# Performance work log

Measured on AMD Instinct MI355X. Metric: run time of the kernel, lower is better.

## Reference

```python
import jax, jax.numpy as jnp
import numpy as np

N_ACT = 300000
C = 128
K = 9
BATCH, H, W = 4, 1024, 1024
EPS = 1e-4  # scn BatchNormalization default eps


def _build_rulebook(rng):
    # sample N_ACT unique active sites on a (BATCH, H, W) grid
    flat = np.sort(rng.choice(BATCH * H * W, size=N_ACT, replace=False).astype(np.int64))
    b = flat // (H * W)
    y = (flat // W) % H
    x = flat % W
    nbr = np.full((N_ACT, K), -1, dtype=np.int32)
    k = 0
    for dy in (-1, 0, 1):
        for dx in (-1, 0, 1):
            ny, nx = y + dy, x + dx
            valid = (ny >= 0) & (ny < H) & (nx >= 0) & (nx < W)
            nflat = b * (H * W) + ny * W + nx
            pos = np.searchsorted(flat, nflat)
            pos_c = np.clip(pos, 0, N_ACT - 1)
            found = valid & (flat[pos_c] == nflat)
            nbr[:, k] = np.where(found, pos_c, -1).astype(np.int32)
            k += 1
    return jnp.asarray(nbr)


def setup_inputs() -> dict:
    key = jax.random.key(0)
    k1, k2, k3 = jax.random.split(key, 3)
    rng = np.random.default_rng(0)
    nbr_idx = _build_rulebook(rng)
    scale = 1.0 / np.sqrt(K * C)
    return {
        "x": jax.random.normal(k1, (N_ACT, C), dtype=jnp.float32),
        "nbr_idx": nbr_idx,
        "W1": jax.random.normal(k2, (K, C, C), dtype=jnp.float32) * scale,
        "gamma1": jnp.ones((C,), jnp.float32),
        "beta1": jnp.zeros((C,), jnp.float32),
        "W2": jax.random.normal(k3, (K, C, C), dtype=jnp.float32) * scale,
        "gamma2": jnp.ones((C,), jnp.float32),
        "beta2": jnp.zeros((C,), jnp.float32),
    }


def _subm_conv(feats, nbr_idx, Wk):
    # gather -> GEMM -> accumulate, one pass per kernel offset (K=9 fixed)
    out = jnp.zeros((feats.shape[0], Wk.shape[2]), feats.dtype)
    for k in range(Wk.shape[0]):
        idx = nbr_idx[:, k]
        mask = (idx >= 0)[:, None]
        g = jnp.where(mask, feats[jnp.maximum(idx, 0)], 0.0)
        out = out + g @ Wk[k]
    return out


def _batchnorm(feats, gamma, beta):
    mean = feats.mean(axis=0)
    var = feats.var(axis=0)  # biased, as in torch BN normalization
    return (feats - mean) * jax.lax.rsqrt(var + EPS) * gamma + beta


def reference(x, nbr_idx, W1, gamma1, beta1, W2, gamma2, beta2):
    out = _subm_conv(x, nbr_idx, W1)
    out = jax.nn.relu(_batchnorm(out, gamma1, beta1))  # BatchNormReLU
    out = _subm_conv(out, nbr_idx, W2)
    out = _batchnorm(out, gamma2, beta2)  # BatchNormalization
    return jax.nn.relu(out + x)  # AddTable + ReLU
```

## Files before the change

### kernel.cpp

```cpp
#include <hip/hip_runtime.h>


#define N_ACT 300000
#define NTAP  9
#define EPSV  1e-4f

using f16x8 = __attribute__((ext_vector_type(8))) _Float16;
using f32x4 = __attribute__((ext_vector_type(4))) float;

#define OFF_PH    0UL
#define OFF_TMP   76800000UL
#define OFF_W1    230400000UL
#define OFF_W2    (OFF_W1 + 294912UL)
#define OFF_STATS (OFF_W2 + 294912UL)
#define OFF_ZBUF  (OFF_STATS + 2048UL)
#define OFF_SB    (OFF_ZBUF + 256UL)

__device__ __forceinline__ unsigned short f2h(float v) {
  _Float16 h = (_Float16)v;
  return __builtin_bit_cast(unsigned short, h);
}

__global__ void prep_kernel(const float* __restrict__ W1, const float* __restrict__ W2,
                            unsigned short* __restrict__ w1, unsigned short* __restrict__ w2,
                            float* __restrict__ zstats) {
  int b = blockIdx.x, t = threadIdx.x;
  if (b == 36) {
    for (int i = t; i < 576; i += 256) zstats[i] = 0.f;
    return;
  }
  int w = b / 18, rem = b % 18;
  int tap = rem >> 1, ch = rem & 1;
  const float* W = w ? W2 : W1;
  unsigned short* o = w ? w2 : w1;
  int n  = t >> 1;
  int s0 = (t & 1) * 4;
  for (int s = s0; s < s0 + 4; ++s) {
    int sigma = s ^ (n & 7);
    for (int j = 0; j < 8; ++j) {
      int   k = ch * 64 + sigma * 8 + j;
      float v = W[tap * 16384 + k * 128 + n];
      o[rem * 8192 + n * 64 + s * 8 + j] = f2h(v);
    }
  }
}

__global__ void tohalf_kernel(const float* __restrict__ x, unsigned short* __restrict__ ph) {
  int i = (blockIdx.x * 256 + threadIdx.x) * 8;
  float4 a = *(const float4*)(x + i);
  float4 b = *(const float4*)(x + i + 4);
  uint4 p;
  p.x = (unsigned)f2h(a.x) | ((unsigned)f2h(a.y) << 16);
  p.y = (unsigned)f2h(a.z) | ((unsigned)f2h(a.w) << 16);
  p.z = (unsigned)f2h(b.x) | ((unsigned)f2h(b.y) << 16);
  p.w = (unsigned)f2h(b.z) | ((unsigned)f2h(b.w) << 16);
  *(uint4*)(ph + i) = p;
}

__global__ __launch_bounds__(256, 2)
void conv_kernel(const unsigned short* __restrict__ pH, const int* __restrict__ nbr,
                 const unsigned short* __restrict__ wH,
                 unsigned short* __restrict__ outp, float* __restrict__ ssum, float* __restrict__ ssq,
                 const unsigned short* __restrict__ zbuf) {
  __shared__ char smem[65536];
  const int t  = threadIdx.x;
  const int wv = t >> 6, ln = t & 63;
  const int m0 = blockIdx.x * 128;
  const int rs = ln >> 3, sg = ln & 7;
  const int lane16 = ln & 15, g = ln >> 4;

  int idx[NTAP][4];
#pragma unroll
  for (int tap = 0; tap < NTAP; ++tap)
#pragma unroll
    for (int it = 0; it < 4; ++it) {
      int gm = m0 + wv * 32 + it * 8 + rs;
      idx[tap][it] = (gm < N_ACT) ? nbr[gm * 9 + tap] : -1;
    }

  f32x4 acc[16];
#pragma unroll
  for (int i = 0; i < 16; ++i) acc[i] = f32x4{0.f, 0.f, 0.f, 0.f};

  auto stage = [&](int c, int p) {
    const int tap = c >> 1, ch = c & 1;
#pragma unroll
    for (int it = 0; it < 4; ++it) {
      int r     = wv * 32 + it * 8 + rs;
      int sigma = sg ^ (r & 7);
      int id    = idx[tap][it];
      long off  = (long)(id >= 0 ? id : 0) * 128 + ch * 64 + sigma * 8;
      const unsigned short* gs = (id >= 0) ? (pH + off) : (zbuf + sigma * 8);
      int lo = p * 16384 + r * 128 + sg * 16;
      __builtin_amdgcn_global_load_lds((const __attribute__((address_space(1))) void*)gs,
                                       (__attribute__((address_space(3))) void*)(smem + lo), 16, 0, 0);
    }
    const char* gb = (const char*)wH + (tap * 2 + ch) * 16384;
#pragma unroll
    for (int it = 0; it < 4; ++it) {
      int o = wv * 4096 + it * 1024 + ln * 16;
      __builtin_amdgcn_global_load_lds((const __attribute__((address_space(1))) void*)(gb + o),
                                       (__attribute__((address_space(3))) void*)(smem + 32768 + p * 16384 + o), 16, 0, 0);
    }
  };

  auto compute = [&](int p) {
    const char* bufA = smem + p * 16384;
    const char* bufB = smem + 32768 + p * 16384;
#pragma unroll
    for (int ks = 0; ks < 2; ++ks) {
      f16x8 ah[4], bh[4];
      int sigma = ks * 4 + g;
#pragma unroll
      for (int mt = 0; mt < 4; ++mt) {
        int m = (wv & 1) * 64 + mt * 16 + lane16;
        ah[mt] = *(const f16x8*)(bufA + m * 128 + ((sigma ^ (m & 7)) * 16));
      }
#pragma unroll
      for (int nt = 0; nt < 4; ++nt) {
        int n = (wv >> 1) * 64 + nt * 16 + lane16;
        bh[nt] = *(const f16x8*)(bufB + n * 128 + ((sigma ^ (n & 7)) * 16));
      }
#pragma unroll
      for (int mt = 0; mt < 4; ++mt)
#pragma unroll
        for (int nt = 0; nt < 4; ++nt)
          acc[mt * 4 + nt] = __builtin_amdgcn_mfma_f32_16x16x32_f16(ah[mt], bh[nt], acc[mt * 4 + nt], 0, 0, 0);
    }
  };

  stage(0, 0);
  asm volatile("s_waitcnt vmcnt(0)" ::: "memory");
  __builtin_amdgcn_sched_barrier(0);
  __builtin_amdgcn_s_barrier();

#pragma unroll
  for (int c = 0; c < 17; ++c) {
    stage(c + 1, (c + 1) & 1);
    compute(c & 1);
    asm volatile("s_waitcnt vmcnt(0)" ::: "memory");
    __builtin_amdgcn_sched_barrier(0);
    __builtin_amdgcn_s_barrier();
  }
  compute(1);

  int rowbase = m0 + (wv & 1) * 64;
  int colbase = (wv >> 1) * 64;
  float s[4], q[4];
#pragma unroll
  for (int nt = 0; nt < 4; ++nt) { s[nt] = 0.f; q[nt] = 0.f; }
#pragma unroll
  for (int mt = 0; mt < 4; ++mt)
#pragma unroll
    for (int nt = 0; nt < 4; ++nt)
#pragma unroll
      for (int r = 0; r < 4; ++r) {
        float v  = acc[mt * 4 + nt][r];
        int  row = rowbase + mt * 16 + g * 4 + r;
        int  col = colbase + nt * 16 + lane16;
        if (row < N_ACT) outp[row * 128 + col] = f2h(v);
        s[nt] += v; q[nt] += v * v;
      }
  __syncthreads();
  float* sbuf = (float*)smem;
  float* qbuf = ((float*)smem) + 256;
#pragma unroll
  for (int nt = 0; nt < 4; ++nt) {
    float sv = s[nt], qv = q[nt];
    sv += __shfl_xor(sv, 16, 64); sv += __shfl_xor(sv, 32, 64);
    qv += __shfl_xor(qv, 16, 64); qv += __shfl_xor(qv, 32, 64);
    if (ln < 16) { sbuf[wv * 64 + nt * 16 + ln] = sv; qbuf[wv * 64 + nt * 16 + ln] = qv; }
  }
  __syncthreads();
  if (t < 128) {
    int c = t;
    float tot = (c < 64) ? (sbuf[c] + sbuf[64 + c]) : (sbuf[128 + (c - 64)] + sbuf[192 + (c - 64)]);
    atomicAdd(ssum + c, tot);
  } else {
    int c = t - 128;
    float tot = (c < 64) ? (qbuf[c] + qbuf[64 + c]) : (qbuf[128 + (c - 64)] + qbuf[192 + (c - 64)]);
    atomicAdd(ssq + c, tot);
  }
}

__global__ void finalize_stats_kernel(const float* __restrict__ ssum, const float* __restrict__ ssq,
                                      const float* __restrict__ gamma, const float* __restrict__ beta,
                                      float* __restrict__ scale, float* __restrict__ bias) {
  int c = threadIdx.x;
  float mean = ssum[c] * (1.f / N_ACT);
  float var  = ssq[c] * (1.f / N_ACT) - mean * mean;
  float sc   = rsqrtf(var + EPSV) * gamma[c];
  scale[c] = sc;
  bias[c]  = beta[c] - mean * sc;
}

__global__ void bn_relu_tohalf_kernel(const unsigned short* __restrict__ tmp,
                                      const float* __restrict__ scale, const float* __restrict__ bias,
                                      unsigned short* __restrict__ ph) {
  int i = (blockIdx.x * 256 + threadIdx.x) * 8;
  int c = i & 127;
  f16x8 v = *(const f16x8*)(tmp + i);
  float4 s0 = *(const float4*)(scale + c);
  float4 s1 = *(const float4*)(scale + c + 4);
  float4 b0 = *(const float4*)(bias + c);
  float4 b1 = *(const float4*)(bias + c + 4);
  float y0 = fmaxf((float)v[0] * s0.x + b0.x, 0.f);
  float y1 = fmaxf((float)v[1] * s0.y + b0.y, 0.f);
  float y2 = fmaxf((float)v[2] * s0.z + b0.z, 0.f);
  float y3 = fmaxf((float)v[3] * s0.w + b0.w, 0.f);
  float y4 = fmaxf((float)v[4] * s1.x + b1.x, 0.f);
  float y5 = fmaxf((float)v[5] * s1.y + b1.y, 0.f);
  float y6 = fmaxf((float)v[6] * s1.z + b1.z, 0.f);
  float y7 = fmaxf((float)v[7] * s1.w + b1.w, 0.f);
  uint4 p;
  p.x = (unsigned)f2h(y0) | ((unsigned)f2h(y1) << 16);
  p.y = (unsigned)f2h(y2) | ((unsigned)f2h(y3) << 16);
  p.z = (unsigned)f2h(y4) | ((unsigned)f2h(y5) << 16);
  p.w = (unsigned)f2h(y6) | ((unsigned)f2h(y7) << 16);
  *(uint4*)(ph + i) = p;
}

__global__ void final_kernel(const unsigned short* __restrict__ tmp,
                             const float* __restrict__ scale, const float* __restrict__ bias,
                             const float* __restrict__ x, float* __restrict__ outp) {
  int i = (blockIdx.x * 256 + threadIdx.x) * 8;
  int c = i & 127;
  f16x8 v = *(const f16x8*)(tmp + i);
  float4 s0 = *(const float4*)(scale + c);
  float4 s1 = *(const float4*)(scale + c + 4);
  float4 b0 = *(const float4*)(bias + c);
  float4 b1 = *(const float4*)(bias + c + 4);
  float4 x0 = *(const float4*)(x + i);
  float4 x1 = *(const float4*)(x + i + 4);
  float4 o0, o1;
  o0.x = fmaxf((float)v[0] * s0.x + b0.x + x0.x, 0.f);
  o0.y = fmaxf((float)v[1] * s0.y + b0.y + x0.y, 0.f);
  o0.z = fmaxf((float)v[2] * s0.z + b0.z + x0.z, 0.f);
  o0.w = fmaxf((float)v[3] * s0.w + b0.w + x0.w, 0.f);
  o1.x = fmaxf((float)v[4] * s1.x + b1.x + x1.x, 0.f);
  o1.y = fmaxf((float)v[5] * s1.y + b1.y + x1.y, 0.f);
  o1.z = fmaxf((float)v[6] * s1.z + b1.z + x1.z, 0.f);
  o1.w = fmaxf((float)v[7] * s1.w + b1.w + x1.w, 0.f);
  *(float4*)(outp + i) = o0;
  *(float4*)(outp + i + 4) = o1;
}

extern "C" void kernel_launch(void* const* d_in, const int* in_sizes, int n_in,
                              void* d_out, int out_size, void* d_ws, size_t ws_size,
                              hipStream_t stream) {
  const float* x   = (const float*)d_in[0];
  const int*   nbr = (const int*)d_in[1];
  const float* W1  = (const float*)d_in[2];
  const float* g1  = (const float*)d_in[3];
  const float* b1  = (const float*)d_in[4];
  const float* W2  = (const float*)d_in[5];
  const float* g2  = (const float*)d_in[6];
  const float* b2  = (const float*)d_in[7];
  float* out = (float*)d_out;
  char*  ws  = (char*)d_ws;

  unsigned short* ph  = (unsigned short*)(ws + OFF_PH);
  unsigned short* tmp = (unsigned short*)(ws + OFF_TMP);
  unsigned short* w1  = (unsigned short*)(ws + OFF_W1);
  unsigned short* w2  = (unsigned short*)(ws + OFF_W2);
  float*          st  = (float*)(ws + OFF_STATS);
  unsigned short* zb  = (unsigned short*)(ws + OFF_ZBUF);
  float*          sc  = (float*)(ws + OFF_SB);
  float*          bi  = sc + 128;

  prep_kernel<<<37, 256, 0, stream>>>(W1, W2, w1, w2, st);
  tohalf_kernel<<<18750, 256, 0, stream>>>(x, ph);
  conv_kernel<<<2344, 256, 0, stream>>>(ph, nbr, w1, tmp, st, st + 128, zb);
  finalize_stats_kernel<<<1, 128, 0, stream>>>(st, st + 128, g1, b1, sc, bi);
  bn_relu_tohalf_kernel<<<18750, 256, 0, stream>>>(tmp, sc, bi, ph);
  conv_kernel<<<2344, 256, 0, stream>>>(ph, nbr, w2, tmp, st + 256, st + 384, zb);
  finalize_stats_kernel<<<1, 128, 0, stream>>>(st + 256, st + 384, g2, b2, sc, bi);
  final_kernel<<<18750, 256, 0, stream>>>(tmp, sc, bi, x, out);
}
```

Measured before the change: 569.9 us.

## Stream weights directly into registers, stage gathers via registers, fuse BN finalize

```diff
diff --git a/kernel.cpp b/kernel.cpp
--- a/kernel.cpp
+++ b/kernel.cpp
@@ -14,7 +14,6 @@
 #define OFF_W2    (OFF_W1 + 294912UL)
 #define OFF_STATS (OFF_W2 + 294912UL)
 #define OFF_ZBUF  (OFF_STATS + 2048UL)
-#define OFF_SB    (OFF_ZBUF + 256UL)
 
 __device__ __forceinline__ unsigned short f2h(float v) {
   _Float16 h = (_Float16)v;
@@ -33,15 +32,15 @@
   int tap = rem >> 1, ch = rem & 1;
   const float* W = w ? W2 : W1;
   unsigned short* o = w ? w2 : w1;
-  int n  = t >> 1;
-  int s0 = (t & 1) * 4;
-  for (int s = s0; s < s0 + 4; ++s) {
-    int sigma = s ^ (n & 7);
-    for (int j = 0; j < 8; ++j) {
-      int   k = ch * 64 + sigma * 8 + j;
-      float v = W[tap * 16384 + k * 128 + n];
-      o[rem * 8192 + n * 64 + s * 8 + j] = f2h(v);
-    }
+  for (int it = 0; it < 4; ++it) {
+    int tp = it * 256 + t;
+    int ln = tp & 63, nt = (tp >> 6) & 3, ks = (tp >> 8) & 1, n6 = tp >> 9;
+    int n     = n6 * 64 + nt * 16 + (ln & 15);
+    int kbase = ch * 64 + (ks * 4 + (ln >> 4)) * 8;
+    unsigned short v8[8];
+    for (int j = 0; j < 8; ++j)
+      v8[j] = f2h(W[tap * 16384 + (kbase + j) * 128 + n]);
+    *(uint4*)(o + rem * 8192 + n6 * 4096 + ks * 2048 + nt * 512 + ln * 8) = *(uint4*)v8;
   }
 }
 
@@ -62,7 +61,7 @@
                  const unsigned short* __restrict__ wH,
                  unsigned short* __restrict__ outp, float* __restrict__ ssum, float* __restrict__ ssq,
                  const unsigned short* __restrict__ zbuf) {
-  __shared__ char smem[65536];
+  __shared__ char smem[32768];
   const int t  = threadIdx.x;
   const int wv = t >> 6, ln = t & 63;
   const int m0 = blockIdx.x * 128;
@@ -82,34 +81,38 @@
 #pragma unroll
   for (int i = 0; i < 16; ++i) acc[i] = f32x4{0.f, 0.f, 0.f, 0.f};
 
-  auto stage = [&](int c, int p) {
+  auto loadA = [&](int c, uint4* dst) {
     const int tap = c >> 1, ch = c & 1;
 #pragma unroll
     for (int it = 0; it < 4; ++it) {
       int r     = wv * 32 + it * 8 + rs;
       int sigma = sg ^ (r & 7);
       int id    = idx[tap][it];
-      long off  = (long)(id >= 0 ? id : 0) * 128 + ch * 64 + sigma * 8;
-      const unsigned short* gs = (id >= 0) ? (pH + off) : (zbuf + sigma * 8);
-      int lo = p * 16384 + r * 128 + sg * 16;
-      __builtin_amdgcn_global_load_lds((const __attribute__((address_space(1))) void*)gs,
-                                       (__attribute__((address_space(3))) void*)(smem + lo), 16, 0, 0);
-    }
-    const char* gb = (const char*)wH + (tap * 2 + ch) * 16384;
+      const unsigned short* gs = (id >= 0) ? (pH + (long)id * 128 + ch * 64 + sigma * 8)
+                                           : (zbuf + sigma * 8);
+      dst[it] = *(const uint4*)gs;
+    }
+  };
+  auto writeA = [&](int p, const uint4* src) {
 #pragma unroll
     for (int it = 0; it < 4; ++it) {
-      int o = wv * 4096 + it * 1024 + ln * 16;
-      __builtin_amdgcn_global_load_lds((const __attribute__((address_space(1))) void*)(gb + o),
-                                       (__attribute__((address_space(3))) void*)(smem + 32768 + p * 16384 + o), 16, 0, 0);
-    }
-  };
-
-  auto compute = [&](int p) {
+      int r = wv * 32 + it * 8 + rs;
+      *(uint4*)(smem + p * 16384 + r * 128 + sg * 16) = src[it];
+    }
+  };
+  auto loadB = [&](int c, f16x8 (*dst)[4]) {
+    const unsigned short* base = wH + c * 8192 + (wv >> 1) * 4096 + ln * 8;
+#pragma unroll
+    for (int ks = 0; ks < 2; ++ks)
+#pragma unroll
+      for (int nt = 0; nt < 4; ++nt)
+        dst[ks][nt] = *(const f16x8*)(base + ks * 2048 + nt * 512);
+  };
+  auto compute = [&](int p, f16x8 (*bh)[4]) {
     const char* bufA = smem + p * 16384;
-    const char* bufB = smem + 32768 + p * 16384;
 #pragma unroll
     for (int ks = 0; ks < 2; ++ks) {
-      f16x8 ah[4], bh[4];
+      f16x8 ah[4];
       int sigma = ks * 4 + g;
 #pragma unroll
       for (int mt = 0; mt < 4; ++mt) {
@@ -117,32 +120,38 @@
         ah[mt] = *(const f16x8*)(bufA + m * 128 + ((sigma ^ (m & 7)) * 16));
       }
 #pragma unroll
-      for (int nt = 0; nt < 4; ++nt) {
-        int n = (wv >> 1) * 64 + nt * 16 + lane16;
-        bh[nt] = *(const f16x8*)(bufB + n * 128 + ((sigma ^ (n & 7)) * 16));
-      }
-#pragma unroll
       for (int mt = 0; mt < 4; ++mt)
 #pragma unroll
         for (int nt = 0; nt < 4; ++nt)
-          acc[mt * 4 + nt] = __builtin_amdgcn_mfma_f32_16x16x32_f16(ah[mt], bh[nt], acc[mt * 4 + nt], 0, 0, 0);
-    }
-  };
-
-  stage(0, 0);
-  asm volatile("s_waitcnt vmcnt(0)" ::: "memory");
-  __builtin_amdgcn_sched_barrier(0);
-  __builtin_amdgcn_s_barrier();
-
-#pragma unroll
-  for (int c = 0; c < 17; ++c) {
-    stage(c + 1, (c + 1) & 1);
-    compute(c & 1);
-    asm volatile("s_waitcnt vmcnt(0)" ::: "memory");
+          acc[mt * 4 + nt] = __builtin_amdgcn_mfma_f32_16x16x32_f16(ah[mt], bh[ks][nt], acc[mt * 4 + nt], 0, 0, 0);
+    }
+  };
+
+  uint4 aR[2][4];
+  f16x8 bR[2][2][4];
+
+  {
+    uint4 a0[4];
+    loadA(0, a0);
+    loadA(1, aR[1]);
+    loadB(0, bR[0]);
+    loadB(1, bR[1]);
+    writeA(0, a0);
+    asm volatile("s_waitcnt lgkmcnt(0)" ::: "memory");
     __builtin_amdgcn_sched_barrier(0);
     __builtin_amdgcn_s_barrier();
   }
-  compute(1);
+#pragma unroll
+  for (int c = 0; c < 17; ++c) {
+    if (c < 16) loadA(c + 2, aR[c & 1]);
+    compute(c & 1, bR[c & 1]);
+    if (c < 16) loadB(c + 2, bR[c & 1]);
+    writeA((c + 1) & 1, aR[(c + 1) & 1]);
+    asm volatile("s_waitcnt lgkmcnt(0)" ::: "memory");
+    __builtin_amdgcn_sched_barrier(0);
+    __builtin_amdgcn_s_barrier();
+  }
+  compute(1, bR[1]);
 
   int rowbase = m0 + (wv & 1) * 64;
   int colbase = (wv >> 1) * 64;
@@ -183,36 +192,30 @@
   }
 }
 
-__global__ void finalize_stats_kernel(const float* __restrict__ ssum, const float* __restrict__ ssq,
+__global__ void bn_relu_tohalf_kernel(const unsigned short* __restrict__ tmp,
+                                      const float* __restrict__ ssum, const float* __restrict__ ssq,
                                       const float* __restrict__ gamma, const float* __restrict__ beta,
-                                      float* __restrict__ scale, float* __restrict__ bias) {
-  int c = threadIdx.x;
-  float mean = ssum[c] * (1.f / N_ACT);
-  float var  = ssq[c] * (1.f / N_ACT) - mean * mean;
-  float sc   = rsqrtf(var + EPSV) * gamma[c];
-  scale[c] = sc;
-  bias[c]  = beta[c] - mean * sc;
-}
-
-__global__ void bn_relu_tohalf_kernel(const unsigned short* __restrict__ tmp,
-                                      const float* __restrict__ scale, const float* __restrict__ bias,
                                       unsigned short* __restrict__ ph) {
   int i = (blockIdx.x * 256 + threadIdx.x) * 8;
   int c = i & 127;
   f16x8 v = *(const f16x8*)(tmp + i);
-  float4 s0 = *(const float4*)(scale + c);
-  float4 s1 = *(const float4*)(scale + c + 4);
-  float4 b0 = *(const float4*)(bias + c);
-  float4 b1 = *(const float4*)(bias + c + 4);
-  float y0 = fmaxf((float)v[0] * s0.x + b0.x, 0.f);
-  float y1 = fmaxf((float)v[1] * s0.y + b0.y, 0.f);
-  float y2 = fmaxf((float)v[2] * s0.z + b0.z, 0.f);
-  float y3 = fmaxf((float)v[3] * s0.w + b0.w, 0.f);
-  float y4 = fmaxf((float)v[4] * s1.x + b1.x, 0.f);
-  float y5 = fmaxf((float)v[5] * s1.y + b1.y, 0.f);
-  float y6 = fmaxf((float)v[6] * s1.z + b1.z, 0.f);
-  float y7 = fmaxf((float)v[7] * s1.w + b1.w, 0.f);
+  float sc[8], bs[8];
+#pragma unroll
+  for (int j = 0; j < 8; ++j) {
+    float mean = ssum[c + j] * (1.f / N_ACT);
+    float var  = ssq[c + j] * (1.f / N_ACT) - mean * mean;
+    float k    = rsqrtf(var + EPSV) * gamma[c + j];
+    sc[j] = k; bs[j] = beta[c + j] - mean * k;
+  }
   uint4 p;
+  float y0 = fmaxf((float)v[0] * sc[0] + bs[0], 0.f);
+  float y1 = fmaxf((float)v[1] * sc[1] + bs[1], 0.f);
+  float y2 = fmaxf((float)v[2] * sc[2] + bs[2], 0.f);
+  float y3 = fmaxf((float)v[3] * sc[3] + bs[3], 0.f);
+  float y4 = fmaxf((float)v[4] * sc[4] + bs[4], 0.f);
+  float y5 = fmaxf((float)v[5] * sc[5] + bs[5], 0.f);
+  float y6 = fmaxf((float)v[6] * sc[6] + bs[6], 0.f);
+  float y7 = fmaxf((float)v[7] * sc[7] + bs[7], 0.f);
   p.x = (unsigned)f2h(y0) | ((unsigned)f2h(y1) << 16);
   p.y = (unsigned)f2h(y2) | ((unsigned)f2h(y3) << 16);
   p.z = (unsigned)f2h(y4) | ((unsigned)f2h(y5) << 16);
@@ -221,26 +224,31 @@
 }
 
 __global__ void final_kernel(const unsigned short* __restrict__ tmp,
-                             const float* __restrict__ scale, const float* __restrict__ bias,
+                             const float* __restrict__ ssum, const float* __restrict__ ssq,
+                             const float* __restrict__ gamma, const float* __restrict__ beta,
                              const float* __restrict__ x, float* __restrict__ outp) {
   int i = (blockIdx.x * 256 + threadIdx.x) * 8;
   int c = i & 127;
   f16x8 v = *(const f16x8*)(tmp + i);
-  float4 s0 = *(const float4*)(scale + c);
-  float4 s1 = *(const float4*)(scale + c + 4);
-  float4 b0 = *(const float4*)(bias + c);
-  float4 b1 = *(const float4*)(bias + c + 4);
+  float sc[8], bs[8];
+#pragma unroll
+  for (int j = 0; j < 8; ++j) {
+    float mean = ssum[c + j] * (1.f / N_ACT);
+    float var  = ssq[c + j] * (1.f / N_ACT) - mean * mean;
+    float k    = rsqrtf(var + EPSV) * gamma[c + j];
+    sc[j] = k; bs[j] = beta[c + j] - mean * k;
+  }
   float4 x0 = *(const float4*)(x + i);
   float4 x1 = *(const float4*)(x + i + 4);
   float4 o0, o1;
-  o0.x = fmaxf((float)v[0] * s0.x + b0.x + x0.x, 0.f);
-  o0.y = fmaxf((float)v[1] * s0.y + b0.y + x0.y, 0.f);
-  o0.z = fmaxf((float)v[2] * s0.z + b0.z + x0.z, 0.f);
-  o0.w = fmaxf((float)v[3] * s0.w + b0.w + x0.w, 0.f);
-  o1.x = fmaxf((float)v[4] * s1.x + b1.x + x1.x, 0.f);
-  o1.y = fmaxf((float)v[5] * s1.y + b1.y + x1.y, 0.f);
-  o1.z = fmaxf((float)v[6] * s1.z + b1.z + x1.z, 0.f);
-  o1.w = fmaxf((float)v[7] * s1.w + b1.w + x1.w, 0.f);
+  o0.x = fmaxf((float)v[0] * sc[0] + bs[0] + x0.x, 0.f);
+  o0.y = fmaxf((float)v[1] * sc[1] + bs[1] + x0.y, 0.f);
+  o0.z = fmaxf((float)v[2] * sc[2] + bs[2] + x0.z, 0.f);
+  o0.w = fmaxf((float)v[3] * sc[3] + bs[3] + x0.w, 0.f);
+  o1.x = fmaxf((float)v[4] * sc[4] + bs[4] + x1.x, 0.f);
+  o1.y = fmaxf((float)v[5] * sc[5] + bs[5] + x1.y, 0.f);
+  o1.z = fmaxf((float)v[6] * sc[6] + bs[6] + x1.z, 0.f);
+  o1.w = fmaxf((float)v[7] * sc[7] + bs[7] + x1.w, 0.f);
   *(float4*)(outp + i) = o0;
   *(float4*)(outp + i + 4) = o1;
 }
@@ -265,15 +273,11 @@
   unsigned short* w2  = (unsigned short*)(ws + OFF_W2);
   float*          st  = (float*)(ws + OFF_STATS);
   unsigned short* zb  = (unsigned short*)(ws + OFF_ZBUF);
-  float*          sc  = (float*)(ws + OFF_SB);
-  float*          bi  = sc + 128;
 
   prep_kernel<<<37, 256, 0, stream>>>(W1, W2, w1, w2, st);
   tohalf_kernel<<<18750, 256, 0, stream>>>(x, ph);
   conv_kernel<<<2344, 256, 0, stream>>>(ph, nbr, w1, tmp, st, st + 128, zb);
-  finalize_stats_kernel<<<1, 128, 0, stream>>>(st, st + 128, g1, b1, sc, bi);
-  bn_relu_tohalf_kernel<<<18750, 256, 0, stream>>>(tmp, sc, bi, ph);
+  bn_relu_tohalf_kernel<<<18750, 256, 0, stream>>>(tmp, st, st + 128, g1, b1, ph);
   conv_kernel<<<2344, 256, 0, stream>>>(ph, nbr, w2, tmp, st + 256, st + 384, zb);
-  finalize_stats_kernel<<<1, 128, 0, stream>>>(st + 256, st + 384, g2, b2, sc, bi);
-  final_kernel<<<18750, 256, 0, stream>>>(tmp, sc, bi, x, out);
-}
+  final_kernel<<<18750, 256, 0, stream>>>(tmp, st + 256, st + 384, g2, b2, x, out);
+}
```

Result: slower. 859.9 us (+50.9%).
